# Performance work log

Measured on AMD Instinct MI355X. Metric: run time of the kernel, lower is better.

## Reference

```python
import jax, jax.numpy as jnp
import numpy as np

EPS = 1e-5
TEMP = 0.07
LARGE_NEG = -1e9


def mi_net(x, W1, g1, b1, W2, b2, Ws, lng, lnb):
    # x: (B, C, T). 1x1 convs == per-position channel projections.
    y = jnp.einsum('bct,oc->bot', x, W1)                      # conv1 (no bias)
    mu = y.mean(axis=(0, 2), keepdims=True)                   # BatchNorm2d, training-mode batch stats
    var = y.var(axis=(0, 2), keepdims=True)
    y = (y - mu) * jax.lax.rsqrt(var + EPS) * g1[None, :, None] + b1[None, :, None]
    y = jax.nn.relu(y)
    y = jnp.einsum('bot,po->bpt', y, W2) + b2[None, :, None]  # conv2 (bias)
    h = y + jnp.einsum('bct,oc->bot', x, Ws)                  # linear shortcut
    mu2 = h.mean(axis=1, keepdims=True)                       # LayerNorm over channel dim
    v2 = h.var(axis=1, keepdims=True)
    return (h - mu2) * jax.lax.rsqrt(v2 + EPS) * lng[None, :, None] + lnb[None, :, None]


def infonce(L, G):
    # L: (N, D, T) locals, G: (N, D) single global per sample (n_multis = 1)
    N, D, T = L.shape
    l_p = jnp.swapaxes(L, 1, 2)                               # (N, T, D)
    l_p = l_p / jnp.linalg.norm(l_p, axis=2, keepdims=True)
    g = G / jnp.linalg.norm(G, axis=1, keepdims=True)         # (N, D)
    u_p = (jnp.einsum('ntd,nd->nt', l_p, g) / TEMP)[:, :, None]   # (N, T, 1), positives scaled by temp
    # negatives: <global_i, local_{j,t}>; NOT divided by temperature (faithful to torch source)
    u_n = jnp.einsum('nd,mtd->nmt', g, l_p)                   # (N, N, T)
    eye = jnp.eye(N, dtype=bool)[:, :, None]
    u_n = jnp.where(eye, LARGE_NEG, u_n).reshape(N, N * T)    # mask self pairs
    logits = jnp.concatenate(
        [u_p, jnp.broadcast_to(u_n[:, None, :], (N, T, N * T))], axis=2)  # (N, T, 1+N*T)
    logp = jax.nn.log_softmax(logits, axis=2)
    return -logp[:, :, 0].mean()


def setup_inputs() -> dict:
    key = jax.random.key(0)
    ks = jax.random.split(key, 10)
    B, CL, CG, T, MI = 32, 1536, 192, 256, 512
    d = {
        'local_feat': jax.random.normal(ks[0], (B, CL, T), jnp.float32),
        'global_feat': jax.random.normal(ks[1], (B, CG), jnp.float32),
        # local_net params
        'lW1': jax.random.normal(ks[2], (MI, CL), jnp.float32) * 0.02,
        'lg1': jnp.ones((MI,), jnp.float32),
        'lb1': jnp.zeros((MI,), jnp.float32),
        'lW2': jax.random.normal(ks[3], (MI, MI), jnp.float32) * 0.02,
        'lb2': jnp.zeros((MI,), jnp.float32),
        'lWs': jax.random.normal(ks[4], (MI, CL), jnp.float32) * 0.02,
        'llng': jnp.ones((MI,), jnp.float32),
        'llnb': jnp.zeros((MI,), jnp.float32),
        # global_net params (global_channels != mi_units -> net exists)
        'gW1': jax.random.normal(ks[5], (MI, CG), jnp.float32) * 0.02,
        'gg1': jnp.ones((MI,), jnp.float32),
        'gb1': jnp.zeros((MI,), jnp.float32),
        'gW2': jax.random.normal(ks[6], (MI, MI), jnp.float32) * 0.02,
        'gb2': jnp.zeros((MI,), jnp.float32),
    }
    # shortcut with near-identity init (n_units >= n_input for global net)
    gWs = jax.random.uniform(ks[7], (MI, CG), jnp.float32, -0.01, 0.01)
    gWs = gWs.at[jnp.arange(CG), jnp.arange(CG)].set(1.0)
    d['gWs'] = gWs
    d['glng'] = jnp.ones((MI,), jnp.float32)
    d['glnb'] = jnp.zeros((MI,), jnp.float32)
    return d


def reference(local_feat, global_feat,
              lW1, lg1, lb1, lW2, lb2, lWs, llng, llnb,
              gW1, gg1, gb1, gW2, gb2, gWs, glng, glnb):
    L = mi_net(local_feat, lW1, lg1, lb1, lW2, lb2, lWs, llng, llnb)      # (B, MI, T)
    G = mi_net(global_feat[:, :, None], gW1, gg1, gb1, gW2, gb2, gWs, glng, glnb)[:, :, 0]  # (B, MI)
    return infonce(L, G)
```

## Files before the change

### kernel.cpp

```cpp
#include <hip/hip_runtime.h>

#define B 32
#define CL 1536
#define CG 192
#define T 256
#define MI 512
#define NPOS 8192
#define EPS 1e-5f
#define TEMP 0.07f

typedef __attribute__((ext_vector_type(8))) __bf16 bf16x8;
typedef __attribute__((ext_vector_type(4))) float f32x4;

__device__ __forceinline__ unsigned short f2bf(float f) {
  union { float f; unsigned u; } v; v.f = f;
  unsigned r = v.u + 0x7FFFu + ((v.u >> 16) & 1u);
  return (unsigned short)(r >> 16);
}
__device__ __forceinline__ float bf2f(unsigned short h) {
  union { unsigned u; float f; } v; v.u = ((unsigned)h) << 16;
  return v.f;
}

__device__ __forceinline__ float wave_sum(float v) {
#pragma unroll
  for (int off = 32; off > 0; off >>= 1) v += __shfl_xor(v, off, 64);
  return v;
}
__device__ __forceinline__ float block_sum(float v, float* rb) {
  v = wave_sum(v);
  __syncthreads();
  if ((threadIdx.x & 63) == 0) rb[threadIdx.x >> 6] = v;
  __syncthreads();
  return rb[0] + rb[1] + rb[2] + rb[3];
}

__global__ __launch_bounds__(256) void k_prep(
    const float* __restrict__ x, const float* __restrict__ lW1,
    const float* __restrict__ lWs, const float* __restrict__ lW2,
    const float* __restrict__ gx, const float* __restrict__ gW1,
    unsigned short* __restrict__ xT, unsigned short* __restrict__ Wc,
    unsigned short* __restrict__ W2b, float* __restrict__ y1g,
    float* __restrict__ bsum) {
  __shared__ float xs[64][65];
  const int bi = blockIdx.x, tid = threadIdx.x;
  if (bi < 1792) {
    int idx = (bi * 256 + tid) * 4;
    const float* src; unsigned short* dst;
    if (idx < 786432) { src = lW1 + idx; dst = Wc + idx; }
    else if (idx < 1572864) { src = lWs + (idx - 786432); dst = Wc + idx; }
    else { src = lW2 + (idx - 1572864); dst = W2b + (idx - 1572864); }
    float4 v = *(const float4*)src;
    ushort4 o = {f2bf(v.x), f2bf(v.y), f2bf(v.z), f2bf(v.w)};
    *(ushort4*)dst = o;
  } else if (bi < 4864) {
    int bi2 = bi - 1792;
    int b = bi2 / 96, rem = bi2 - b * 96;
    int c0 = (rem >> 2) * 64, t0 = (rem & 3) * 64;
    const float* xb = x + ((size_t)b * CL + c0) * T + t0;
#pragma unroll
    for (int i = 0; i < 16; i++) {
      int idx = tid + i * 256, c = idx >> 6, t = idx & 63;
      xs[c][t] = xb[(size_t)c * T + t];
    }
    __syncthreads();
    unsigned short* ob = xT + ((size_t)b * T + t0) * CL + c0;
#pragma unroll
    for (int half = 0; half < 2; half++) {
      int s = tid + half * 256;
      int t = s >> 3, kg = s & 7;
      unsigned short v[8];
#pragma unroll
      for (int j = 0; j < 8; j++) v[j] = f2bf(xs[kg * 8 + j][t]);
      uint4 o = {(unsigned)v[0] | ((unsigned)v[1] << 16),
                 (unsigned)v[2] | ((unsigned)v[3] << 16),
                 (unsigned)v[4] | ((unsigned)v[5] << 16),
                 (unsigned)v[6] | ((unsigned)v[7] << 16)};
      *(uint4*)&ob[(size_t)t * CL + kg * 8] = o;
    }
  } else if (bi < 4928) {
    int idx = (bi - 4864) * 256 + tid;
    int b = idx & 31, o = idx >> 5;
    float s = 0.f;
    for (int c = 0; c < CG; c++) s = fmaf(gx[b * CG + c], gW1[o * CG + c], s);
    y1g[o * 32 + b] = s;
  } else {
    float4 z = {0.f, 0.f, 0.f, 0.f};
    ((float4*)bsum)[tid] = z;
  }
}

__global__ __launch_bounds__(256, 2) void k_gemm1(
    const unsigned short* __restrict__ xT, const unsigned short* __restrict__ Wc,
    unsigned short* __restrict__ y1u, unsigned short* __restrict__ ysb,
    float* __restrict__ bsum, float* __restrict__ bsq,
    const float* __restrict__ y1g, const float* __restrict__ gg1,
    const float* __restrict__ gb1, const float* __restrict__ gW2,
    const float* __restrict__ gb2, const float* __restrict__ gx,
    const float* __restrict__ gWsc, float* __restrict__ hg) {
  const int tid = threadIdx.x, bi = blockIdx.x;
  if (bi >= 512) {
    __shared__ float gsc[512], gsh[512];
#pragma unroll
    for (int jj = 0; jj < 2; jj++) {
      int o = tid + jj * 256;
      float s = 0.f, s2 = 0.f;
      for (int b = 0; b < 32; b++) {
        float v = y1g[o * 32 + b];
        s += v; s2 = fmaf(v, v, s2);
      }
      float mu = s * (1.f / 32.f);
      float var = s2 * (1.f / 32.f) - mu * mu;
      float sc = gg1[o] * rsqrtf(var + EPS);
      gsc[o] = sc;
      gsh[o] = gb1[o] - mu * sc;
    }
    __syncthreads();
    int idx = (bi - 512) * 256 + tid;
    int b = idx & 31, p = idx >> 5;
    float s = gb2[p];
    for (int o = 0; o < MI; o++) {
      float v = fmaxf(fmaf(y1g[o * 32 + b], gsc[o], gsh[o]), 0.f);
      s = fmaf(v, gW2[(size_t)p * MI + o], s);
    }
    for (int c = 0; c < CG; c++) s = fmaf(gx[b * CG + c], gWsc[p * CG + c], s);
    hg[p * 32 + b] = s;
    return;
  }
  __shared__ __align__(16) unsigned short As[128 * 64];
  __shared__ __align__(16) unsigned short Bs[128 * 64];
  const int w = tid >> 6, lane = tid & 63;
  const int m0 = (bi & 63) * 128, o0 = (bi >> 6) * 128;
  const int wm = w & 1, wn = w >> 1;
  const int lm = lane & 15, q = lane >> 4;
  const int drow = lane >> 3;
  const int dchunk = (lane & 7) ^ drow;
  const int swz = lm & 7;
  f32x4 acc[4][4];
#pragma unroll
  for (int i = 0; i < 4; i++)
#pragma unroll
    for (int j = 0; j < 4; j++) acc[i][j] = f32x4{0.f, 0.f, 0.f, 0.f};

  const unsigned short* pa = xT + (size_t)(m0 + w * 32 + drow) * CL + dchunk * 8;
  const unsigned short* pb = Wc + (size_t)(o0 + w * 32 + drow) * CL + dchunk * 8;
  for (int k0 = 0; k0 < CL; k0 += 64) {
#pragma unroll
    for (int i = 0; i < 4; i++) {
      __builtin_amdgcn_global_load_lds(
          (const __attribute__((address_space(1))) void*)(pa + (size_t)i * 8 * CL + k0),
          (__attribute__((address_space(3))) void*)&As[(w * 32 + i * 8) * 64], 16, 0, 0);
      __builtin_amdgcn_global_load_lds(
          (const __attribute__((address_space(1))) void*)(pb + (size_t)i * 8 * CL + k0),
          (__attribute__((address_space(3))) void*)&Bs[(w * 32 + i * 8) * 64], 16, 0, 0);
    }
    __syncthreads();
#pragma unroll
    for (int kc = 0; kc < 2; kc++) {
      const int col = (((kc * 4 + q) ^ swz)) * 8;
      bf16x8 af[4], bfr[4];
#pragma unroll
      for (int mi = 0; mi < 4; mi++)
        af[mi] = *(const bf16x8*)&As[(wm * 64 + mi * 16 + lm) * 64 + col];
#pragma unroll
      for (int ni = 0; ni < 4; ni++)
        bfr[ni] = *(const bf16x8*)&Bs[(wn * 64 + ni * 16 + lm) * 64 + col];
#pragma unroll
      for (int mi = 0; mi < 4; mi++)
#pragma unroll
        for (int ni = 0; ni < 4; ni++)
          acc[mi][ni] = __builtin_amdgcn_mfma_f32_16x16x32_bf16(
              af[mi], bfr[ni], acc[mi][ni], 0, 0, 0);
    }
    __syncthreads();
  }
  const int row0 = m0 + wm * 64 + q * 4;
  const bool isY1 = (o0 < 512);
  unsigned short* dst = isY1 ? y1u : ysb;
  const int ob = isY1 ? o0 : o0 - 512;
#pragma unroll
  for (int mi = 0; mi < 4; mi++)
#pragma unroll
    for (int ni = 0; ni < 4; ni++) {
      int oc = ob + wn * 64 + ni * 16 + lm;
#pragma unroll
      for (int r = 0; r < 4; r++)
        dst[(size_t)(row0 + mi * 16 + r) * 512 + oc] = f2bf(acc[mi][ni][r]);
    }
  if (isY1) {
#pragma unroll
    for (int ni = 0; ni < 4; ni++) {
      float s = 0.f, s2 = 0.f;
#pragma unroll
      for (int mi = 0; mi < 4; mi++)
#pragma unroll
        for (int r = 0; r < 4; r++) {
          float v = acc[mi][ni][r];
          s += v; s2 = fmaf(v, v, s2);
        }
      s += __shfl_xor(s, 16, 64);  s2 += __shfl_xor(s2, 16, 64);
      s += __shfl_xor(s, 32, 64);  s2 += __shfl_xor(s2, 32, 64);
      if (q == 0) {
        int c = o0 + wn * 64 + ni * 16 + lm;
        atomicAdd(&bsum[c], s);
        atomicAdd(&bsq[c], s2);
      }
    }
  }
}

__global__ __launch_bounds__(256) void k_bnapp(
    const unsigned short* __restrict__ y1u, const float* __restrict__ bsum,
    const float* __restrict__ bsq, const float* __restrict__ lg1,
    const float* __restrict__ lb1, unsigned short* __restrict__ vv,
    const float* __restrict__ hg, const float* __restrict__ glng,
    const float* __restrict__ glnb, unsigned short* __restrict__ gnormb) {
  __shared__ float rb[4];
  const int bi = blockIdx.x, tid = threadIdx.x;
  if (bi >= 4096) {
    int b = bi - 4096;
    float v0 = hg[tid * 32 + b];
    float v1 = hg[(tid + 256) * 32 + b];
    float s = block_sum(v0 + v1, rb);
    float s2 = block_sum(fmaf(v0, v0, v1 * v1), rb);
    float mu = s * (1.f / MI);
    float var = s2 * (1.f / MI) - mu * mu;
    float rstd = rsqrtf(var + EPS);
    float L0 = fmaf((v0 - mu) * rstd, glng[tid], glnb[tid]);
    float L1 = fmaf((v1 - mu) * rstd, glng[tid + 256], glnb[tid + 256]);
    float n2 = block_sum(fmaf(L0, L0, L1 * L1), rb);
    float inv = rsqrtf(n2);
    gnormb[b * MI + tid] = f2bf(L0 * inv);
    gnormb[b * MI + tid + 256] = f2bf(L1 * inv);
    return;
  }
  int idx = (bi * 256 + tid) * 4;
  int o = idx & 511;
  ushort4 in = *(const ushort4*)&y1u[idx];
  float iv[4] = {bf2f(in.x), bf2f(in.y), bf2f(in.z), bf2f(in.w)};
  unsigned short ov[4];
#pragma unroll
  for (int j = 0; j < 4; j++) {
    float mu = bsum[o + j] * (1.f / NPOS);
    float var = bsq[o + j] * (1.f / NPOS) - mu * mu;
    float sc = lg1[o + j] * rsqrtf(var + EPS);
    float sh = lb1[o + j] - mu * sc;
    ov[j] = f2bf(fmaxf(fmaf(iv[j], sc, sh), 0.f));
  }
  ushort4 out = {ov[0], ov[1], ov[2], ov[3]};
  *(ushort4*)&vv[idx] = out;
}

__global__ __launch_bounds__(256, 2) void k_gemm2(
    const unsigned short* __restrict__ vv, const unsigned short* __restrict__ W2b,
    const float* __restrict__ b2, unsigned short* __restrict__ hb16) {
  __shared__ __align__(16) unsigned short As[128 * 64];
  __shared__ __align__(16) unsigned short Bs[128 * 64];
  const int tid = threadIdx.x, bi = blockIdx.x;
  const int w = tid >> 6, lane = tid & 63;
  const int m0 = (bi & 63) * 128, p0 = (bi >> 6) * 128;
  const int wm = w & 1, wn = w >> 1;
  const int lm = lane & 15, q = lane >> 4;
  const int drow = lane >> 3;
  const int dchunk = (lane & 7) ^ drow;
  const int swz = lm & 7;
  f32x4 acc[4][4];
#pragma unroll
  for (int i = 0; i < 4; i++)
#pragma unroll
    for (int j = 0; j < 4; j++) acc[i][j] = f32x4{0.f, 0.f, 0.f, 0.f};

  const unsigned short* pa = vv + (size_t)(m0 + w * 32 + drow) * 512 + dchunk * 8;
  const unsigned short* pb = W2b + (size_t)(p0 + w * 32 + drow) * 512 + dchunk * 8;
  for (int k0 = 0; k0 < 512; k0 += 64) {
#pragma unroll
    for (int i = 0; i < 4; i++) {
      __builtin_amdgcn_global_load_lds(
          (const __attribute__((address_space(1))) void*)(pa + (size_t)i * 8 * 512 + k0),
          (__attribute__((address_space(3))) void*)&As[(w * 32 + i * 8) * 64], 16, 0, 0);
      __builtin_amdgcn_global_load_lds(
          (const __attribute__((address_space(1))) void*)(pb + (size_t)i * 8 * 512 + k0),
          (__attribute__((address_space(3))) void*)&Bs[(w * 32 + i * 8) * 64], 16, 0, 0);
    }
    __syncthreads();
#pragma unroll
    for (int kc = 0; kc < 2; kc++) {
      const int col = (((kc * 4 + q) ^ swz)) * 8;
      bf16x8 af[4], bfr[4];
#pragma unroll
      for (int mi = 0; mi < 4; mi++)
        af[mi] = *(const bf16x8*)&As[(wm * 64 + mi * 16 + lm) * 64 + col];
#pragma unroll
      for (int ni = 0; ni < 4; ni++)
        bfr[ni] = *(const bf16x8*)&Bs[(wn * 64 + ni * 16 + lm) * 64 + col];
#pragma unroll
      for (int mi = 0; mi < 4; mi++)
#pragma unroll
        for (int ni = 0; ni < 4; ni++)
          acc[mi][ni] = __builtin_amdgcn_mfma_f32_16x16x32_bf16(
              af[mi], bfr[ni], acc[mi][ni], 0, 0, 0);
    }
    __syncthreads();
  }
  const int row0 = m0 + wm * 64 + q * 4;
#pragma unroll
  for (int ni = 0; ni < 4; ni++) {
    int p = p0 + wn * 64 + ni * 16 + lm;
    float bias = b2[p];
#pragma unroll
    for (int mi = 0; mi < 4; mi++)
#pragma unroll
      for (int r = 0; r < 4; r++) {
        size_t off = (size_t)(row0 + mi * 16 + r) * 512 + p;
        hb16[off] = f2bf(acc[mi][ni][r] + bias);
      }
  }
}

__global__ __launch_bounds__(256) void k_tail(
    const unsigned short* __restrict__ hb16, const unsigned short* __restrict__ ysb,
    const float* __restrict__ lng, const float* __restrict__ lnb,
    const unsigned short* __restrict__ gnormb,
    float* __restrict__ up, float* __restrict__ pmax, float* __restrict__ psum) {
  __shared__ __align__(16) unsigned short gs[32 * 512];
  __shared__ __align__(16) unsigned short Ls[32 * 512];
  __shared__ float Ured[4 * 1024];
  const int tid = threadIdx.x;
  const int w = tid >> 6, lane = tid & 63;
  const int r0 = blockIdx.x * 32;
  const int smp = r0 >> 8;
#pragma unroll
  for (int i = 0; i < 8; i++) {
    int e = (tid + i * 256) * 8;
    *(uint4*)&gs[e] = *(const uint4*)&gnormb[e];
  }
  float4 g0 = *(const float4*)&lng[lane * 8];
  float4 g1 = *(const float4*)&lng[lane * 8 + 4];
  float4 bb0 = *(const float4*)&lnb[lane * 8];
  float4 bb1 = *(const float4*)&lnb[lane * 8 + 4];
  float gg[8] = {g0.x, g0.y, g0.z, g0.w, g1.x, g1.y, g1.z, g1.w};
  float bz[8] = {bb0.x, bb0.y, bb0.z, bb0.w, bb1.x, bb1.y, bb1.z, bb1.w};
#pragma unroll
  for (int j = 0; j < 8; j++) {
    int rr = w * 8 + j;
    size_t off = (size_t)(r0 + rr) * 512 + lane * 8;
    uint4 hu = *(const uint4*)&hb16[off];
    uint4 yu = *(const uint4*)&ysb[off];
    unsigned short hv[8] = {
        (unsigned short)(hu.x & 0xffff), (unsigned short)(hu.x >> 16),
        (unsigned short)(hu.y & 0xffff), (unsigned short)(hu.y >> 16),
        (unsigned short)(hu.z & 0xffff), (unsigned short)(hu.z >> 16),
        (unsigned short)(hu.w & 0xffff), (unsigned short)(hu.w >> 16)};
    unsigned short yv[8] = {
        (unsigned short)(yu.x & 0xffff), (unsigned short)(yu.x >> 16),
        (unsigned short)(yu.y & 0xffff), (unsigned short)(yu.y >> 16),
        (unsigned short)(yu.z & 0xffff), (unsigned short)(yu.z >> 16),
        (unsigned short)(yu.w & 0xffff), (unsigned short)(yu.w >> 16)};
    float v[8];
    float s = 0.f, s2 = 0.f;
#pragma unroll
    for (int k = 0; k < 8; k++) {
      v[k] = bf2f(hv[k]) + bf2f(yv[k]);
      s += v[k]; s2 = fmaf(v[k], v[k], s2);
    }
    s = wave_sum(s);
    s2 = wave_sum(s2);
    float mu = s * (1.f / MI);
    float var = s2 * (1.f / MI) - mu * mu;
    float rstd = rsqrtf(var + EPS);
    float L[8], n2 = 0.f;
#pragma unroll
    for (int k = 0; k < 8; k++) {
      L[k] = fmaf((v[k] - mu) * rstd, gg[k], bz[k]);
      n2 = fmaf(L[k], L[k], n2);
    }
    n2 = wave_sum(n2);
    float inv = rsqrtf(n2);
    unsigned short* orow = &Ls[rr * 512 + lane * 8];
    ushort4 o0 = {f2bf(L[0] * inv), f2bf(L[1] * inv), f2bf(L[2] * inv), f2bf(L[3] * inv)};
    ushort4 o1 = {f2bf(L[4] * inv), f2bf(L[5] * inv), f2bf(L[6] * inv), f2bf(L[7] * inv)};
    *(ushort4*)orow = o0;
    *(ushort4*)(orow + 4) = o1;
  }
  __syncthreads();
  const int lm = lane & 15, q = lane >> 4;
  f32x4 acc[2][2];
#pragma unroll
  for (int i = 0; i < 2; i++)
#pragma unroll
    for (int j = 0; j < 2; j++) acc[i][j] = f32x4{0.f, 0.f, 0.f, 0.f};
#pragma unroll
  for (int kk = 0; kk < 4; kk++) {
    int k0 = w * 128 + kk * 32 + q * 8;
    bf16x8 af[2], bfr[2];
#pragma unroll
    for (int mi = 0; mi < 2; mi++)
      af[mi] = *(const bf16x8*)&gs[(mi * 16 + lm) * 512 + k0];
#pragma unroll
    for (int ni = 0; ni < 2; ni++)
      bfr[ni] = *(const bf16x8*)&Ls[(ni * 16 + lm) * 512 + k0];
#pragma unroll
    for (int mi = 0; mi < 2; mi++)
#pragma unroll
      for (int ni = 0; ni < 2; ni++)
        acc[mi][ni] = __builtin_amdgcn_mfma_f32_16x16x32_bf16(
            af[mi], bfr[ni], acc[mi][ni], 0, 0, 0);
  }
#pragma unroll
  for (int mi = 0; mi < 2; mi++)
#pragma unroll
    for (int ni = 0; ni < 2; ni++)
#pragma unroll
      for (int r = 0; r < 4; r++) {
        int m = mi * 16 + q * 4 + r, n = ni * 16 + lm;
        Ured[w * 1024 + m * 32 + n] = acc[mi][ni][r];
      }
  __syncthreads();
  float u[4];
#pragma unroll
  for (int j = 0; j < 4; j++) {
    int idx = tid * 4 + j;
    u[j] = Ured[idx] + Ured[1024 + idx] + Ured[2048 + idx] + Ured[3072 + idx];
  }
  __syncthreads();
#pragma unroll
  for (int j = 0; j < 4; j++) Ured[tid * 4 + j] = u[j];
  int m = (tid * 4) >> 5;
  if (m == smp) {
#pragma unroll
    for (int j = 0; j < 4; j++)
      up[r0 + ((tid * 4 + j) & 31)] = u[j] * (1.f / TEMP);
  }
  __syncthreads();
  if (tid < 32) {
    float mx = -1e30f, s = 0.f;
    if (tid != smp) {
      for (int n = 0; n < 32; n++) mx = fmaxf(mx, Ured[tid * 32 + n]);
      for (int n = 0; n < 32; n++) s += expf(Ured[tid * 32 + n] - mx);
    }
    pmax[tid * 256 + blockIdx.x] = mx;
    psum[tid * 256 + blockIdx.x] = s;
  }
}

__global__ __launch_bounds__(256) void k_loss(
    const float* __restrict__ up, const float* __restrict__ pmax,
    const float* __restrict__ psum, float* __restrict__ out) {
  __shared__ float rb[4];
  __shared__ float red[32][8];
  __shared__ float Ms[32], Ss[32];
  const int tid = threadIdx.x;
  const int n = tid >> 3, j = tid & 7;
  float mx = -1e30f;
  for (int c = j * 32; c < j * 32 + 32; c++) mx = fmaxf(mx, pmax[n * 256 + c]);
  red[n][j] = mx;
  __syncthreads();
  if (j == 0) {
    float M = -1e30f;
#pragma unroll
    for (int k = 0; k < 8; k++) M = fmaxf(M, red[n][k]);
    Ms[n] = M;
  }
  __syncthreads();
  float M = Ms[n];
  float s = 0.f;
  for (int c = j * 32; c < j * 32 + 32; c++)
    s += psum[n * 256 + c] * expf(pmax[n * 256 + c] - M);
  __syncthreads();
  red[n][j] = s;
  __syncthreads();
  if (j == 0) {
    float S = 0.f;
#pragma unroll
    for (int k = 0; k < 8; k++) S += red[n][k];
    Ss[n] = S;
  }
  __syncthreads();
  float acc = 0.f;
  for (int i = tid; i < NPOS; i += 256) {
    int nn = i >> 8;
    float upv = up[i];
    float Mn = Ms[nn], Sn = Ss[nn];
    float mx2 = fmaxf(upv, Mn);
    float lse = mx2 + logf(expf(upv - mx2) + Sn * expf(Mn - mx2));
    acc += lse - upv;
  }
  acc = block_sum(acc, rb);
  if (tid == 0) out[0] = acc * (1.f / NPOS);
}

extern "C" void kernel_launch(void* const* d_in, const int* in_sizes, int n_in,
                              void* d_out, int out_size, void* d_ws, size_t ws_size,
                              hipStream_t stream) {
  (void)in_sizes; (void)n_in; (void)out_size; (void)ws_size;
  const float* x    = (const float*)d_in[0];
  const float* gx   = (const float*)d_in[1];
  const float* lW1  = (const float*)d_in[2];
  const float* lg1  = (const float*)d_in[3];
  const float* lb1  = (const float*)d_in[4];
  const float* lW2  = (const float*)d_in[5];
  const float* lb2  = (const float*)d_in[6];
  const float* lWs  = (const float*)d_in[7];
  const float* llng = (const float*)d_in[8];
  const float* llnb = (const float*)d_in[9];
  const float* gW1  = (const float*)d_in[10];
  const float* gg1  = (const float*)d_in[11];
  const float* gb1  = (const float*)d_in[12];
  const float* gW2  = (const float*)d_in[13];
  const float* gb2  = (const float*)d_in[14];
  const float* gWs  = (const float*)d_in[15];
  const float* glng = (const float*)d_in[16];
  const float* glnb = (const float*)d_in[17];

  char* wsb = (char*)d_ws;
  unsigned short* xT     = (unsigned short*)(wsb);
  unsigned short* Wc     = (unsigned short*)(wsb + 25165824);
  unsigned short* W2b    = (unsigned short*)(wsb + 28311552);
  unsigned short* y1u    = (unsigned short*)(wsb + 28835840);
  unsigned short* ysb    = (unsigned short*)(wsb + 37224448);
  unsigned short* vv     = (unsigned short*)(wsb + 45613056);
  unsigned short* hb16   = (unsigned short*)(wsb + 54001664);
  float* bsum            = (float*)(wsb + 62390272);
  float* bsq             = (float*)(wsb + 62392320);
  float* y1g             = (float*)(wsb + 62394368);
  float* hg              = (float*)(wsb + 62459904);
  unsigned short* gnormb = (unsigned short*)(wsb + 62525440);
  float* up              = (float*)(wsb + 62558208);
  float* pmax            = (float*)(wsb + 62590976);
  float* psum            = (float*)(wsb + 62623744);

  k_prep<<<dim3(4929), 256, 0, stream>>>(x, lW1, lWs, lW2, gx, gW1, xT, Wc, W2b,
                                         y1g, bsum);
  k_gemm1<<<dim3(576), 256, 0, stream>>>(xT, Wc, y1u, ysb, bsum, bsq,
                                         y1g, gg1, gb1, gW2, gb2, gx, gWs, hg);
  k_bnapp<<<dim3(4128), 256, 0, stream>>>(y1u, bsum, bsq, lg1, lb1, vv,
                                          hg, glng, glnb, gnormb);
  k_gemm2<<<dim3(256), 256, 0, stream>>>(vv, W2b, lb2, hb16);
  k_tail<<<dim3(256), 256, 0, stream>>>(hb16, ysb, llng, llnb, gnormb,
                                        up, pmax, psum);
  k_loss<<<dim3(1), 256, 0, stream>>>(up, pmax, psum, (float*)d_out);
}
```

Before: 217.2 us.

## Fuse BN-apply into GEMM2 A-load and fold loss into tail via last-block counter

Removes the separate batchnorm-apply kernel by computing per-channel scale/shift in k_gemm2 and applying BN+ReLU while staging the A tile into LDS with register loads instead of async global-to-LDS loads. The global LayerNorm blocks move into k_gemm2's extra 32 blocks. The single-block loss kernel is folded into k_tail using an atomic counter so the last-finishing block does the final reduction. The x transpose load in k_prep is also vectorised to float4. This saves the vv round trip through memory and two launches, but the A-operand path loses async loads and may expose more latency in the GEMM.

```diff
diff --git a/kernel.cpp b/kernel.cpp
--- a/kernel.cpp
+++ b/kernel.cpp
@@ -41,8 +41,8 @@
     const float* __restrict__ gx, const float* __restrict__ gW1,
     unsigned short* __restrict__ xT, unsigned short* __restrict__ Wc,
     unsigned short* __restrict__ W2b, float* __restrict__ y1g,
-    float* __restrict__ bsum) {
-  __shared__ float xs[64][65];
+    float* __restrict__ bsum, unsigned* __restrict__ counter) {
+  __shared__ float xs[64][68];
   const int bi = blockIdx.x, tid = threadIdx.x;
   if (bi < 1792) {
     int idx = (bi * 256 + tid) * 4;
@@ -59,9 +59,10 @@
     int c0 = (rem >> 2) * 64, t0 = (rem & 3) * 64;
     const float* xb = x + ((size_t)b * CL + c0) * T + t0;
 #pragma unroll
-    for (int i = 0; i < 16; i++) {
-      int idx = tid + i * 256, c = idx >> 6, t = idx & 63;
-      xs[c][t] = xb[(size_t)c * T + t];
+    for (int i = 0; i < 4; i++) {
+      int idx = tid + i * 256, c = idx >> 4, t4 = idx & 15;
+      float4 v = *(const float4*)&xb[(size_t)c * T + t4 * 4];
+      *(float4*)&xs[c][t4 * 4] = v;
     }
     __syncthreads();
     unsigned short* ob = xT + ((size_t)b * T + t0) * CL + c0;
@@ -87,6 +88,7 @@
   } else {
     float4 z = {0.f, 0.f, 0.f, 0.f};
     ((float4*)bsum)[tid] = z;
+    if (tid == 0) counter[0] = 0u;
   }
 }
 
@@ -209,16 +211,17 @@
   }
 }
 
-__global__ __launch_bounds__(256) void k_bnapp(
-    const unsigned short* __restrict__ y1u, const float* __restrict__ bsum,
-    const float* __restrict__ bsq, const float* __restrict__ lg1,
-    const float* __restrict__ lb1, unsigned short* __restrict__ vv,
+__global__ __launch_bounds__(256, 2) void k_gemm2(
+    const unsigned short* __restrict__ y1u, const unsigned short* __restrict__ W2b,
+    const float* __restrict__ bsum, const float* __restrict__ bsq,
+    const float* __restrict__ lg1, const float* __restrict__ lb1,
+    const float* __restrict__ b2, unsigned short* __restrict__ hb16,
     const float* __restrict__ hg, const float* __restrict__ glng,
     const float* __restrict__ glnb, unsigned short* __restrict__ gnormb) {
   __shared__ float rb[4];
-  const int bi = blockIdx.x, tid = threadIdx.x;
-  if (bi >= 4096) {
-    int b = bi - 4096;
+  const int tid = threadIdx.x, bi = blockIdx.x;
+  if (bi >= 256) {
+    int b = bi - 256;
     float v0 = hg[tid * 32 + b];
     float v1 = hg[(tid + 256) * 32 + b];
     float s = block_sum(v0 + v1, rb);
@@ -234,29 +237,9 @@
     gnormb[b * MI + tid + 256] = f2bf(L1 * inv);
     return;
   }
-  int idx = (bi * 256 + tid) * 4;
-  int o = idx & 511;
-  ushort4 in = *(const ushort4*)&y1u[idx];
-  float iv[4] = {bf2f(in.x), bf2f(in.y), bf2f(in.z), bf2f(in.w)};
-  unsigned short ov[4];
-#pragma unroll
-  for (int j = 0; j < 4; j++) {
-    float mu = bsum[o + j] * (1.f / NPOS);
-    float var = bsq[o + j] * (1.f / NPOS) - mu * mu;
-    float sc = lg1[o + j] * rsqrtf(var + EPS);
-    float sh = lb1[o + j] - mu * sc;
-    ov[j] = f2bf(fmaxf(fmaf(iv[j], sc, sh), 0.f));
-  }
-  ushort4 out = {ov[0], ov[1], ov[2], ov[3]};
-  *(ushort4*)&vv[idx] = out;
-}
-
-__global__ __launch_bounds__(256, 2) void k_gemm2(
-    const unsigned short* __restrict__ vv, const unsigned short* __restrict__ W2b,
-    const float* __restrict__ b2, unsigned short* __restrict__ hb16) {
   __shared__ __align__(16) unsigned short As[128 * 64];
   __shared__ __align__(16) unsigned short Bs[128 * 64];
-  const int tid = threadIdx.x, bi = blockIdx.x;
+  __shared__ float scl[512], shf[512];
   const int w = tid >> 6, lane = tid & 63;
   const int m0 = (bi & 63) * 128, p0 = (bi >> 6) * 128;
   const int wm = w & 1, wn = w >> 1;
@@ -264,23 +247,53 @@
   const int drow = lane >> 3;
   const int dchunk = (lane & 7) ^ drow;
   const int swz = lm & 7;
+#pragma unroll
+  for (int jj = 0; jj < 2; jj++) {
+    int ch = tid + jj * 256;
+    float mu = bsum[ch] * (1.f / NPOS);
+    float var = bsq[ch] * (1.f / NPOS) - mu * mu;
+    float sc = lg1[ch] * rsqrtf(var + EPS);
+    scl[ch] = sc;
+    shf[ch] = lb1[ch] - mu * sc;
+  }
+  __syncthreads();
   f32x4 acc[4][4];
 #pragma unroll
   for (int i = 0; i < 4; i++)
 #pragma unroll
     for (int j = 0; j < 4; j++) acc[i][j] = f32x4{0.f, 0.f, 0.f, 0.f};
 
-  const unsigned short* pa = vv + (size_t)(m0 + w * 32 + drow) * 512 + dchunk * 8;
+  const int achk = tid & 7, arow0 = tid >> 3;
   const unsigned short* pb = W2b + (size_t)(p0 + w * 32 + drow) * 512 + dchunk * 8;
   for (int k0 = 0; k0 < 512; k0 += 64) {
 #pragma unroll
-    for (int i = 0; i < 4; i++) {
-      __builtin_amdgcn_global_load_lds(
-          (const __attribute__((address_space(1))) void*)(pa + (size_t)i * 8 * 512 + k0),
-          (__attribute__((address_space(3))) void*)&As[(w * 32 + i * 8) * 64], 16, 0, 0);
+    for (int i = 0; i < 4; i++)
       __builtin_amdgcn_global_load_lds(
           (const __attribute__((address_space(1))) void*)(pb + (size_t)i * 8 * 512 + k0),
           (__attribute__((address_space(3))) void*)&Bs[(w * 32 + i * 8) * 64], 16, 0, 0);
+    float sv[8], hv[8];
+    *(float4*)&sv[0] = *(const float4*)&scl[k0 + achk * 8];
+    *(float4*)&sv[4] = *(const float4*)&scl[k0 + achk * 8 + 4];
+    *(float4*)&hv[0] = *(const float4*)&shf[k0 + achk * 8];
+    *(float4*)&hv[4] = *(const float4*)&shf[k0 + achk * 8 + 4];
+#pragma unroll
+    for (int pass = 0; pass < 4; pass++) {
+      int row = arow0 + pass * 32;
+      uint4 u = *(const uint4*)&y1u[(size_t)(m0 + row) * 512 + k0 + achk * 8];
+      unsigned short iv[8] = {
+          (unsigned short)(u.x & 0xffff), (unsigned short)(u.x >> 16),
+          (unsigned short)(u.y & 0xffff), (unsigned short)(u.y >> 16),
+          (unsigned short)(u.z & 0xffff), (unsigned short)(u.z >> 16),
+          (unsigned short)(u.w & 0xffff), (unsigned short)(u.w >> 16)};
+      unsigned short ov[8];
+#pragma unroll
+      for (int j = 0; j < 8; j++)
+        ov[j] = f2bf(fmaxf(fmaf(bf2f(iv[j]), sv[j], hv[j]), 0.f));
+      uint4 o = {(unsigned)ov[0] | ((unsigned)ov[1] << 16),
+                 (unsigned)ov[2] | ((unsigned)ov[3] << 16),
+                 (unsigned)ov[4] | ((unsigned)ov[5] << 16),
+                 (unsigned)ov[6] | ((unsigned)ov[7] << 16)};
+      *(uint4*)&As[row * 64 + ((achk ^ (row & 7)) * 8)] = o;
     }
     __syncthreads();
 #pragma unroll
@@ -321,10 +334,15 @@
     const unsigned short* __restrict__ hb16, const unsigned short* __restrict__ ysb,
     const float* __restrict__ lng, const float* __restrict__ lnb,
     const unsigned short* __restrict__ gnormb,
-    float* __restrict__ up, float* __restrict__ pmax, float* __restrict__ psum) {
+    float* __restrict__ up, float* __restrict__ pmax, float* __restrict__ psum,
+    unsigned* __restrict__ counter, float* __restrict__ out) {
   __shared__ __align__(16) unsigned short gs[32 * 512];
   __shared__ __align__(16) unsigned short Ls[32 * 512];
   __shared__ float Ured[4 * 1024];
+  __shared__ float rb[4];
+  __shared__ float red2[32][8];
+  __shared__ float Ms[32], Ss[32];
+  __shared__ unsigned isLast;
   const int tid = threadIdx.x;
   const int w = tid >> 6, lane = tid & 63;
   const int r0 = blockIdx.x * 32;
@@ -441,52 +459,54 @@
     pmax[tid * 256 + blockIdx.x] = mx;
     psum[tid * 256 + blockIdx.x] = s;
   }
-}
-
-__global__ __launch_bounds__(256) void k_loss(
-    const float* __restrict__ up, const float* __restrict__ pmax,
-    const float* __restrict__ psum, float* __restrict__ out) {
-  __shared__ float rb[4];
-  __shared__ float red[32][8];
-  __shared__ float Ms[32], Ss[32];
-  const int tid = threadIdx.x;
-  const int n = tid >> 3, j = tid & 7;
-  float mx = -1e30f;
-  for (int c = j * 32; c < j * 32 + 32; c++) mx = fmaxf(mx, pmax[n * 256 + c]);
-  red[n][j] = mx;
-  __syncthreads();
-  if (j == 0) {
-    float M = -1e30f;
-#pragma unroll
-    for (int k = 0; k < 8; k++) M = fmaxf(M, red[n][k]);
-    Ms[n] = M;
-  }
-  __syncthreads();
-  float M = Ms[n];
-  float s = 0.f;
-  for (int c = j * 32; c < j * 32 + 32; c++)
-    s += psum[n * 256 + c] * expf(pmax[n * 256 + c] - M);
-  __syncthreads();
-  red[n][j] = s;
-  __syncthreads();
-  if (j == 0) {
-    float S = 0.f;
-#pragma unroll
-    for (int k = 0; k < 8; k++) S += red[n][k];
-    Ss[n] = S;
-  }
-  __syncthreads();
-  float acc = 0.f;
-  for (int i = tid; i < NPOS; i += 256) {
-    int nn = i >> 8;
-    float upv = up[i];
-    float Mn = Ms[nn], Sn = Ss[nn];
-    float mx2 = fmaxf(upv, Mn);
-    float lse = mx2 + logf(expf(upv - mx2) + Sn * expf(Mn - mx2));
-    acc += lse - upv;
-  }
-  acc = block_sum(acc, rb);
-  if (tid == 0) out[0] = acc * (1.f / NPOS);
+  __threadfence();
+  __syncthreads();
+  if (tid == 0) {
+    unsigned v = atomicAdd(counter, 1u);
+    isLast = (v == 255u) ? 1u : 0u;
+  }
+  __syncthreads();
+  if (!isLast) return;
+  __threadfence();
+  {
+    const int n = tid >> 3, j = tid & 7;
+    float mx = -1e30f;
+    for (int c = j * 32; c < j * 32 + 32; c++) mx = fmaxf(mx, pmax[n * 256 + c]);
+    red2[n][j] = mx;
+    __syncthreads();
+    if (j == 0) {
+      float M = -1e30f;
+#pragma unroll
+      for (int k = 0; k < 8; k++) M = fmaxf(M, red2[n][k]);
+      Ms[n] = M;
+    }
+    __syncthreads();
+    float M = Ms[n];
+    float s = 0.f;
+    for (int c = j * 32; c < j * 32 + 32; c++)
+      s += psum[n * 256 + c] * expf(pmax[n * 256 + c] - M);
+    __syncthreads();
+    red2[n][j] = s;
+    __syncthreads();
+    if (j == 0) {
+      float S = 0.f;
+#pragma unroll
+      for (int k = 0; k < 8; k++) S += red2[n][k];
+      Ss[n] = S;
+    }
+    __syncthreads();
+    float accv = 0.f;
+    for (int i = tid; i < NPOS; i += 256) {
+      int nn = i >> 8;
+      float upv = up[i];
+      float Mn = Ms[nn], Sn = Ss[nn];
+      float mx2 = fmaxf(upv, Mn);
+      float lse = mx2 + logf(expf(upv - mx2) + Sn * expf(Mn - mx2));
+      accv += lse - upv;
+    }
+    accv = block_sum(accv, rb);
+    if (tid == 0) out[0] = accv * (1.f / NPOS);
+  }
 }
 
 extern "C" void kernel_launch(void* const* d_in, const int* in_sizes, int n_in,
@@ -518,7 +538,6 @@
   unsigned short* W2b    = (unsigned short*)(wsb + 28311552);
   unsigned short* y1u    = (unsigned short*)(wsb + 28835840);
   unsigned short* ysb    = (unsigned short*)(wsb + 37224448);
-  unsigned short* vv     = (unsigned short*)(wsb + 45613056);
   unsigned short* hb16   = (unsigned short*)(wsb + 54001664);
   float* bsum            = (float*)(wsb + 62390272);
   float* bsq             = (float*)(wsb + 62392320);
@@ -528,15 +547,14 @@
   float* up              = (float*)(wsb + 62558208);
   float* pmax            = (float*)(wsb + 62590976);
   float* psum            = (float*)(wsb + 62623744);
+  unsigned* counter      = (unsigned*)(wsb + 62656512);
 
   k_prep<<<dim3(4929), 256, 0, stream>>>(x, lW1, lWs, lW2, gx, gW1, xT, Wc, W2b,
-                                         y1g, bsum);
+                                         y1g, bsum, counter);
   k_gemm1<<<dim3(576), 256, 0, stream>>>(xT, Wc, y1u, ysb, bsum, bsq,
                                          y1g, gg1, gb1, gW2, gb2, gx, gWs, hg);
-  k_bnapp<<<dim3(4128), 256, 0, stream>>>(y1u, bsum, bsq, lg1, lb1, vv,
-                                          hg, glng, glnb, gnormb);
-  k_gemm2<<<dim3(256), 256, 0, stream>>>(vv, W2b, lb2, hb16);
+  k_gemm2<<<dim3(288), 256, 0, stream>>>(y1u, W2b, bsum, bsq, lg1, lb1, lb2,
+                                         hb16, hg, glng, glnb, gnormb);
   k_tail<<<dim3(256), 256, 0, stream>>>(hb16, ysb, llng, llnb, gnormb,
-                                        up, pmax, psum);
-  k_loss<<<dim3(1), 256, 0, stream>>>(up, pmax, psum, (float*)d_out);
-}
+                                        up, pmax, psum, counter, (float*)d_out);
+}
```

Result: slower. 235.7 us (+8.5%).
